# Kernel tuning notes

Measured on AMD Instinct MI355X. Metric: run time of the kernel, lower is better.

The kernel has to match this reference:

```python
import jax, jax.numpy as jnp
import numpy as np

B, W, M, HD, RL, RD = 32, 32, 1024, 64, 2, 32
D = RL * HD  # concat of per-layer hidden states


def setup_inputs() -> dict:
    key = jax.random.key(0)
    ks = jax.random.split(key, 16)
    s = 0.1
    r = lambda k, shape: (jax.random.normal(k, shape, jnp.float32) * s)
    return {
        "x_input": jax.random.normal(ks[0], (B, W, M), jnp.float32),
        "major_graph": jax.random.normal(ks[1], (M, M), jnp.float32) * 0.02,
        "H_init": jnp.zeros((RL, M, HD), jnp.float32),
        # GRU layer 0: input size 1 -> hidden HD
        "Wih0": r(ks[2], (3 * HD, 1)),
        "Whh0": r(ks[3], (3 * HD, HD)),
        "bih0": jnp.zeros((3 * HD,), jnp.float32),
        "bhh0": jnp.zeros((3 * HD,), jnp.float32),
        # GRU layer 1: hidden HD -> hidden HD
        "Wih1": r(ks[4], (3 * HD, HD)),
        "Whh1": r(ks[5], (3 * HD, HD)),
        "bih1": jnp.zeros((3 * HD,), jnp.float32),
        "bhh1": jnp.zeros((3 * HD,), jnp.float32),
        # weight-normed Linear(RL*HD -> RD)
        "V": r(ks[6], (RD, D)),
        "g": jnp.ones((RD,), jnp.float32),
        "b_lin": jnp.zeros((RD,), jnp.float32),
        # FinalRowWise layer: per-node weights [M, RD] -> scalar per node
        "W_fr": r(ks[7], (M, RD)),
        "b_fr": jnp.zeros((M,), jnp.float32),
    }


def _gru_cell(x, h, Wih, Whh, bih, bhh):
    # x: [B, M, in], h: [B, M, HD]
    gi = x @ Wih.T + bih
    gh = h @ Whh.T + bhh
    ir, iz, inn = jnp.split(gi, 3, axis=-1)
    hr, hz, hnn = jnp.split(gh, 3, axis=-1)
    rgate = jax.nn.sigmoid(ir + hr)
    zgate = jax.nn.sigmoid(iz + hz)
    n = jnp.tanh(inn + rgate * hnn)
    return (1.0 - zgate) * n + zgate * h


def reference(x_input, major_graph, H_init, Wih0, Whh0, bih0, bhh0,
              Wih1, Whh1, bih1, bhh1, V, g, b_lin, W_fr, b_fr):
    Bn, Wn_, Mn = x_input.shape
    # h0: [RL, B, M, HD] (H_init broadcast over batch)
    h0 = jnp.broadcast_to(H_init[:, None], (H_init.shape[0], Bn, Mn, H_init.shape[-1]))
    # weight_norm (dim=0): per-output-row normalization of V scaled by g
    Wn = g[:, None] * V / jnp.linalg.norm(V, axis=1, keepdims=True)  # [RD, D]
    x_seq = jnp.transpose(x_input, (1, 0, 2))[..., None]  # [W, B, M, 1]

    def step(hn, x_t):
        hn0 = _gru_cell(x_t, hn, Wih0, Whh0, bih0, bhh0)        # [B, M, HD]
        hn1 = _gru_cell(hn0, h0[1], Wih1, Whh1, bih1, bhh1)     # [B, M, HD] (fresh h0 each step, as in source)
        x_p = jnp.concatenate([hn0, hn1], axis=-1)              # [B, M, D]
        # graph-weighted projection along node axis: x_p @ major_graph
        x_g = jax.nn.relu(jnp.einsum('bid,ij->bjd', x_p, major_graph))  # [B, M, D]
        y = jax.nn.sigmoid(x_g @ Wn.T + b_lin)                  # [B, M, RD]
        out = jnp.einsum('bmd,md->bm', y, W_fr) + b_fr          # [B, M]
        return hn1, out

    _, outs = jax.lax.scan(step, h0[0], x_seq)  # [W, B, M]
    return jnp.transpose(outs, (1, 0, 2))       # [B, W, M]
```

## Files before the change

kernel.cpp:

```cpp
#include <hip/hip_runtime.h>
#include <math.h>

#define B_  32
#define W_  32
#define M_  1024
#define HD_ 64
#define RD_ 32
#define D_  128
#define CH_ 16
#define NKT 16

typedef short bf16x8 __attribute__((ext_vector_type(8)));
typedef float f32x4  __attribute__((ext_vector_type(4)));

#define AS1 __attribute__((address_space(1)))
#define AS3 __attribute__((address_space(3)))

__device__ __forceinline__ void gload16(const void* g, void* l) {
    __builtin_amdgcn_global_load_lds((const AS1 void*)g, (AS3 void*)l, 16, 0, 0);
}

__device__ __forceinline__ unsigned short f2b(float f) {
    unsigned int u = __float_as_uint(f);
    u += 0x7fffu + ((u >> 16) & 1u);
    return (unsigned short)(u >> 16);
}
__device__ __forceinline__ float b2f(unsigned short h) {
    return __uint_as_float(((unsigned int)h) << 16);
}
__device__ __forceinline__ float sigf(float x) { return 1.0f / (1.0f + __expf(-x)); }
__device__ __forceinline__ float tanhf_(float x) { return 2.0f / (1.0f + __expf(-2.0f * x)) - 1.0f; }


__global__ __launch_bounds__(256) void gt_kernel(const float* __restrict__ G,
                                                 unsigned short* __restrict__ GTb) {
    __shared__ float T[64][65];
    int i0 = blockIdx.x * 64, j0 = blockIdx.y * 64;
    int tid = threadIdx.x;
    int r = tid >> 4, c4 = (tid & 15) * 4;
    #pragma unroll
    for (int q = 0; q < 4; ++q) {
        float4 v = *(const float4*)&G[(i0 + r + q * 16) * M_ + j0 + c4];
        T[r + q * 16][c4] = v.x; T[r + q * 16][c4 + 1] = v.y;
        T[r + q * 16][c4 + 2] = v.z; T[r + q * 16][c4 + 3] = v.w;
    }
    __syncthreads();
    #pragma unroll
    for (int q = 0; q < 4; ++q) {
        int jr = r + q * 16;
        ushort4 o;
        o.x = f2b(T[c4][jr]); o.y = f2b(T[c4 + 1][jr]);
        o.z = f2b(T[c4 + 2][jr]); o.w = f2b(T[c4 + 3][jr]);
        *(ushort4*)&GTb[(j0 + jr) * M_ + i0 + c4] = o;
    }
}

__global__ __launch_bounds__(192) void gh1ct_kernel(const float* __restrict__ H_init,
                                                    const float* __restrict__ Whh1,
                                                    const float* __restrict__ bhh1,
                                                    float* __restrict__ gh1cT) {
    int m = blockIdx.x, k = threadIdx.x;
    __shared__ float h01[HD_];
    if (k < HD_) h01[k] = H_init[(M_ + m) * HD_ + k];
    __syncthreads();
    float d = 0.f;
    #pragma unroll
    for (int hd = 0; hd < HD_; ++hd) d = fmaf(h01[hd], Whh1[k * HD_ + hd], d);
    gh1cT[k * M_ + m] = d + bhh1[k];
}

__global__ __launch_bounds__(128) void wn_kernel(const float* __restrict__ V,
                                                 const float* __restrict__ g,
                                                 unsigned short* __restrict__ Wnb) {
    int r = blockIdx.x, d = threadIdx.x;
    float v = V[r * D_ + d];
    float s = v * v;
    #pragma unroll
    for (int off = 32; off > 0; off >>= 1) s += __shfl_down(s, off);
    __shared__ float ws[2];
    if ((threadIdx.x & 63) == 0) ws[threadIdx.x >> 6] = s;
    __syncthreads();
    float norm = sqrtf(ws[0] + ws[1]);
    Wnb[r * D_ + d] = f2b(g[r] * v / norm);
}

__global__ __launch_bounds__(256) void castw_kernel(const float* __restrict__ Whh0,
                                                    const float* __restrict__ Wih1,
                                                    unsigned short* __restrict__ Whh0b,
                                                    unsigned short* __restrict__ Wih1b) {
    int i = blockIdx.x * 256 + threadIdx.x;
    Whh0b[i] = f2b(Whh0[i]);
    Wih1b[i] = f2b(Wih1[i]);
}

__global__ __launch_bounds__(256) void inith_kernel(const float* __restrict__ H_init,
                                                    unsigned short* __restrict__ Hb) {
    int e8 = blockIdx.x * 256 + threadIdx.x;
    int base = e8 * 8;
    int src = base & (M_ * HD_ - 1);
    float4 v0 = *(const float4*)&H_init[src];
    float4 v1 = *(const float4*)&H_init[src + 4];
    uint4 u;
    u.x = (unsigned int)f2b(v0.x) | ((unsigned int)f2b(v0.y) << 16);
    u.y = (unsigned int)f2b(v0.z) | ((unsigned int)f2b(v0.w) << 16);
    u.z = (unsigned int)f2b(v1.x) | ((unsigned int)f2b(v1.y) << 16);
    u.w = (unsigned int)f2b(v1.z) | ((unsigned int)f2b(v1.w) << 16);
    *(uint4*)&Hb[base] = u;
}

__global__ __launch_bounds__(512, 4) void gru_chunk_kernel(
    const float* __restrict__ x_input, const float* __restrict__ Wih0,
    const float* __restrict__ bih0, const float* __restrict__ bhh0,
    const unsigned short* __restrict__ Whh0b, const unsigned short* __restrict__ Wih1b,
    const float* __restrict__ bih1, const float* __restrict__ gh1cT,
    const float* __restrict__ H_init, unsigned short* __restrict__ Hb,
    unsigned short* __restrict__ XPT_c, int t0)
{
    __shared__ unsigned short Whh0s[192 * 64];
    __shared__ unsigned short Wih1s[192 * 64];
    __shared__ unsigned short hn0s[64 * 64];
    __shared__ unsigned short hn1s[64 * 64];
    const int tid = threadIdx.x, w = tid >> 6, l = tid & 63;
    const int li = l & 15, lh = l >> 4;
    const int pg = w >> 1, hf = w & 1;
    const int b = blockIdx.x >> 4, mt = blockIdx.x & 15;
    const int m0 = mt * 64;
    const int p0b = b * M_ + m0;
    const int ms = m0 + pg * 16;

    for (int i = tid; i < 1536; i += 512) {
        int row = i >> 3, pos = i & 7, sc = pos ^ (row & 7);
        gload16(&Whh0b[row * 64 + sc * 8], (char*)Whh0s + (i & ~63) * 16);
        gload16(&Wih1b[row * 64 + sc * 8], (char*)Wih1s + (i & ~63) * 16);
    }
    {
        int p = tid >> 3, cc = tid & 7;
        uint4 v = *(const uint4*)&Hb[(p0b + p) * HD_ + cc * 8];
        *(uint4*)((char*)hn1s + p * 128 + ((cc ^ (p & 7)) << 4)) = v;
    }

    float wi_[3][2], bi0_[3][2], bh0_[3][2], bi1_[3][2];
    float vrA[2][4], vzA[2][4], vnA[2][4], h01A[2][4];
    #pragma unroll
    for (int fi = 0; fi < 2; ++fi) {
        int ko = hf * 32 + fi * 16 + li;
        #pragma unroll
        for (int g3 = 0; g3 < 3; ++g3) {
            wi_[g3][fi]  = Wih0[g3 * 64 + ko];
            bi0_[g3][fi] = bih0[g3 * 64 + ko];
            bh0_[g3][fi] = bhh0[g3 * 64 + ko];
            bi1_[g3][fi] = bih1[g3 * 64 + ko];
        }
        float4 vr = *(const float4*)&gh1cT[(ko) * M_ + ms + lh * 4];
        float4 vz = *(const float4*)&gh1cT[(64 + ko) * M_ + ms + lh * 4];
        float4 vn = *(const float4*)&gh1cT[(128 + ko) * M_ + ms + lh * 4];
        vrA[fi][0] = vr.x; vrA[fi][1] = vr.y; vrA[fi][2] = vr.z; vrA[fi][3] = vr.w;
        vzA[fi][0] = vz.x; vzA[fi][1] = vz.y; vzA[fi][2] = vz.z; vzA[fi][3] = vz.w;
        vnA[fi][0] = vn.x; vnA[fi][1] = vn.y; vnA[fi][2] = vn.z; vnA[fi][3] = vn.w;
        #pragma unroll
        for (int reg = 0; reg < 4; ++reg)
            h01A[fi][reg] = H_init[M_ * HD_ + (ms + lh * 4 + reg) * HD_ + ko];
    }

    __syncthreads();

    float hst[2][4];
    #pragma unroll
    for (int fi = 0; fi < 2; ++fi) {
        int ko = hf * 32 + fi * 16 + li;
        #pragma unroll
        for (int reg = 0; reg < 4; ++reg) {
            int ml = pg * 16 + lh * 4 + reg;
            hst[fi][reg] = b2f(*(const unsigned short*)((char*)hn1s + ml * 128 +
                               ((((ko >> 3) ^ (ml & 7))) << 4) + (ko & 7) * 2));
        }
    }

    for (int ts = 0; ts < CH_; ++ts) {
        int t = t0 + ts;
        float4 xv = *(const float4*)&x_input[(b * W_ + t) * M_ + ms + lh * 4];
        float x4[4] = {xv.x, xv.y, xv.z, xv.w};
        const int rl = pg * 16 + li;

        bf16x8 a0 = *(const bf16x8*)((char*)hn1s + rl * 128 + ((lh ^ (rl & 7)) << 4));
        bf16x8 a1 = *(const bf16x8*)((char*)hn1s + rl * 128 + (((4 + lh) ^ (rl & 7)) << 4));
        f32x4 acc[6];
        #pragma unroll
        for (int q = 0; q < 6; ++q) acc[q] = (f32x4){0.f, 0.f, 0.f, 0.f};
        #pragma unroll
        for (int g3 = 0; g3 < 3; ++g3)
            #pragma unroll
            for (int fi = 0; fi < 2; ++fi) {
                int row = (g3 * 4 + hf * 2 + fi) * 16 + li;
                bf16x8 b0 = *(const bf16x8*)((char*)Whh0s + row * 128 + ((lh ^ (row & 7)) << 4));
                bf16x8 b1 = *(const bf16x8*)((char*)Whh0s + row * 128 + (((4 + lh) ^ (row & 7)) << 4));
                acc[g3 * 2 + fi] = __builtin_amdgcn_mfma_f32_16x16x32_bf16(a0, b0, acc[g3 * 2 + fi], 0, 0, 0);
                acc[g3 * 2 + fi] = __builtin_amdgcn_mfma_f32_16x16x32_bf16(a1, b1, acc[g3 * 2 + fi], 0, 0, 0);
            }
        #pragma unroll
        for (int fi = 0; fi < 2; ++fi) {
            int j = hf * 32 + fi * 16 + li;
            #pragma unroll
            for (int reg = 0; reg < 4; ++reg) {
                int ml = pg * 16 + lh * 4 + reg;
                float x = x4[reg];
                float r = sigf(x * wi_[0][fi] + bi0_[0][fi] + acc[fi][reg]     + bh0_[0][fi]);
                float z = sigf(x * wi_[1][fi] + bi0_[1][fi] + acc[2 + fi][reg] + bh0_[1][fi]);
                float n = tanhf_(x * wi_[2][fi] + bi0_[2][fi] + r * (acc[4 + fi][reg] + bh0_[2][fi]));
                float h0v = (1.f - z) * n + z * hst[fi][reg];
                *(unsigned short*)((char*)hn0s + ml * 128 +
                    ((((j >> 3) ^ (ml & 7))) << 4) + (j & 7) * 2) = f2b(h0v);
            }
        }
        __syncthreads();

        a0 = *(const bf16x8*)((char*)hn0s + rl * 128 + ((lh ^ (rl & 7)) << 4));
        a1 = *(const bf16x8*)((char*)hn0s + rl * 128 + (((4 + lh) ^ (rl & 7)) << 4));
        #pragma unroll
        for (int q = 0; q < 6; ++q) acc[q] = (f32x4){0.f, 0.f, 0.f, 0.f};
        #pragma unroll
        for (int g3 = 0; g3 < 3; ++g3)
            #pragma unroll
            for (int fi = 0; fi < 2; ++fi) {
                int row = (g3 * 4 + hf * 2 + fi) * 16 + li;
                bf16x8 b0 = *(const bf16x8*)((char*)Wih1s + row * 128 + ((lh ^ (row & 7)) << 4));
                bf16x8 b1 = *(const bf16x8*)((char*)Wih1s + row * 128 + (((4 + lh) ^ (row & 7)) << 4));
                acc[g3 * 2 + fi] = __builtin_amdgcn_mfma_f32_16x16x32_bf16(a0, b0, acc[g3 * 2 + fi], 0, 0, 0);
                acc[g3 * 2 + fi] = __builtin_amdgcn_mfma_f32_16x16x32_bf16(a1, b1, acc[g3 * 2 + fi], 0, 0, 0);
            }
        #pragma unroll
        for (int fi = 0; fi < 2; ++fi) {
            int ko = hf * 32 + fi * 16 + li;
            #pragma unroll
            for (int reg = 0; reg < 4; ++reg) {
                int ml = pg * 16 + lh * 4 + reg;
                float r = sigf(acc[fi][reg]     + bi1_[0][fi] + vrA[fi][reg]);
                float z = sigf(acc[2 + fi][reg] + bi1_[1][fi] + vzA[fi][reg]);
                float n = tanhf_(acc[4 + fi][reg] + bi1_[2][fi] + r * vnA[fi][reg]);
                float h1v = (1.f - z) * n + z * h01A[fi][reg];
                hst[fi][reg] = h1v;
                *(unsigned short*)((char*)hn1s + ml * 128 +
                    ((((ko >> 3) ^ (ml & 7))) << 4) + (ko & 7) * 2) = f2b(h1v);
            }
        }
        __syncthreads();

        {
            unsigned short* XPT = XPT_c + (size_t)ts * (D_ * B_ * M_);
            int d = tid >> 2, mh = (tid & 3) * 16;
            const char* src = (d < 64) ? (const char*)hn0s : (const char*)hn1s;
            int dd = d & 63;
            unsigned int pk[8];
            #pragma unroll
            for (int mm = 0; mm < 16; mm += 2) {
                int ma = mh + mm, mb = mh + mm + 1;
                unsigned int ua = *(const unsigned short*)(src + ma * 128 + (((dd >> 3) ^ (ma & 7)) << 4) + (dd & 7) * 2);
                unsigned int ub = *(const unsigned short*)(src + mb * 128 + (((dd >> 3) ^ (mb & 7)) << 4) + (dd & 7) * 2);
                pk[mm >> 1] = ua | (ub << 16);
            }
            uint4 o0 = {pk[0], pk[1], pk[2], pk[3]};
            uint4 o1 = {pk[4], pk[5], pk[6], pk[7]};
            *(uint4*)&XPT[(b * D_ + d) * M_ + m0 + mh]     = o0;
            *(uint4*)&XPT[(b * D_ + d) * M_ + m0 + mh + 8] = o1;
        }
        __syncthreads();
    }

    {
        int p = tid >> 3, cc = tid & 7;
        uint4 v = *(const uint4*)((char*)hn1s + p * 128 + ((cc ^ (p & 7)) << 4));
        *(uint4*)&Hb[(p0b + p) * HD_ + cc * 8] = v;
    }
}

__global__ __launch_bounds__(512, 4) void gemmhead_kernel(
    const unsigned short* __restrict__ GTb, const unsigned short* __restrict__ XPT_c,
    const unsigned short* __restrict__ Wnb, const float* __restrict__ b_lin,
    const float* __restrict__ W_fr, const float* __restrict__ b_fr,
    float* __restrict__ out, int t0)
{
    __shared__ __align__(16) char lds[65536];
    const int tid = threadIdx.x, w = tid >> 6, l = tid & 63;
    const int li = l & 15, lh = l >> 4;
    const int wm = w >> 2, wn = w & 3;
    const int bid = blockIdx.x;
    const int ntile = (bid & 7) + ((bid >> 6) << 3);
    const int j0 = ((bid >> 3) & 7) * 128;
    const unsigned short* Asrc = GTb + (size_t)j0 * M_;
    const unsigned short* Bsrc = XPT_c + (size_t)ntile * 128 * M_;

    f32x4 acc[4][2];
    #pragma unroll
    for (int mi = 0; mi < 4; ++mi)
        #pragma unroll
        for (int ni = 0; ni < 2; ++ni) acc[mi][ni] = (f32x4){0.f, 0.f, 0.f, 0.f};

    #define STAGE(kt, c) { \
        _Pragma("unroll") \
        for (int q = 0; q < 2; ++q) { \
            int i = q * 512 + tid; \
            int row = i >> 3, pos = i & 7, sc = pos ^ (row & 7); \
            gload16(&Asrc[row * M_ + (kt) * 64 + sc * 8], lds + (c) * 32768 + (i & ~63) * 16); \
            gload16(&Bsrc[row * M_ + (kt) * 64 + sc * 8], lds + (c) * 32768 + 16384 + (i & ~63) * 16); \
        } }

    STAGE(0, 0);

    for (int kt = 0; kt < NKT; ++kt) {
        if (kt + 1 < NKT) { STAGE(kt + 1, (kt + 1) & 1);
                            asm volatile("s_waitcnt vmcnt(4)" ::: "memory"); }
        else              { asm volatile("s_waitcnt vmcnt(0)" ::: "memory"); }
        __builtin_amdgcn_s_barrier();
        asm volatile("" ::: "memory");
        const char* Abuf = lds + (kt & 1) * 32768;
        const char* Bbuf = Abuf + 16384;
        bf16x8 af[4][2], bfv[2][2];
        #pragma unroll
        for (int mi = 0; mi < 4; ++mi) {
            int row = wm * 64 + mi * 16 + li;
            #pragma unroll
            for (int kk = 0; kk < 2; ++kk)
                af[mi][kk] = *(const bf16x8*)(Abuf + row * 128 + (((kk * 4 + lh) ^ (row & 7)) << 4));
        }
        #pragma unroll
        for (int ni = 0; ni < 2; ++ni) {
            int row = wn * 32 + ni * 16 + li;
            #pragma unroll
            for (int kk = 0; kk < 2; ++kk)
                bfv[ni][kk] = *(const bf16x8*)(Bbuf + row * 128 + (((kk * 4 + lh) ^ (row & 7)) << 4));
        }
        __builtin_amdgcn_s_setprio(1);
        #pragma unroll
        for (int kk = 0; kk < 2; ++kk)
            #pragma unroll
            for (int mi = 0; mi < 4; ++mi)
                #pragma unroll
                for (int ni = 0; ni < 2; ++ni)
                    acc[mi][ni] = __builtin_amdgcn_mfma_f32_16x16x32_bf16(af[mi][kk], bfv[ni][kk], acc[mi][ni], 0, 0, 0);
        __builtin_amdgcn_s_setprio(0);
        asm volatile("s_waitcnt lgkmcnt(0)" ::: "memory");
        __builtin_amdgcn_s_barrier();
        asm volatile("" ::: "memory");
    }

    __syncthreads();

    #pragma unroll
    for (int mi = 0; mi < 4; ++mi)
        #pragma unroll
        for (int ni = 0; ni < 2; ++ni)
            #pragma unroll
            for (int reg = 0; reg < 4; ++reg) {
                int jl = wm * 64 + mi * 16 + lh * 4 + reg;
                int cl = wn * 32 + ni * 16 + li;
                float v = fmaxf(acc[mi][ni][reg], 0.f);
                int byte = jl * 256 + ((((cl >> 3) ^ (jl & 7))) << 4) + (cl & 7) * 2;
                *(unsigned short*)(lds + byte) = f2b(v);
            }
    __syncthreads();

    const int b = ntile & 31, t = t0 + (ntile >> 5);
    float bl0 = b_lin[li], bl1 = b_lin[16 + li];
    {
        int row = w * 16 + li;
        f32x4 P0 = (f32x4){0.f, 0.f, 0.f, 0.f};
        f32x4 P1 = (f32x4){0.f, 0.f, 0.f, 0.f};
        #pragma unroll
        for (int ks = 0; ks < 4; ++ks) {
            int cp = (ks * 4 + lh) ^ (row & 7);
            bf16x8 xa = *(const bf16x8*)(lds + row * 256 + cp * 16);
            bf16x8 wb0 = *(const bf16x8*)&Wnb[(li) * D_ + ks * 32 + lh * 8];
            bf16x8 wb1 = *(const bf16x8*)&Wnb[(16 + li) * D_ + ks * 32 + lh * 8];
            P0 = __builtin_amdgcn_mfma_f32_16x16x32_bf16(xa, wb0, P0, 0, 0, 0);
            P1 = __builtin_amdgcn_mfma_f32_16x16x32_bf16(xa, wb1, P1, 0, 0, 0);
        }
        float s[4];
        #pragma unroll
        for (int reg = 0; reg < 4; ++reg) {
            int j = j0 + w * 16 + lh * 4 + reg;
            float y0 = sigf(P0[reg] + bl0);
            float y1 = sigf(P1[reg] + bl1);
            s[reg] = y0 * W_fr[j * RD_ + li] + y1 * W_fr[j * RD_ + 16 + li];
        }
        #pragma unroll
        for (int off = 1; off < 16; off <<= 1) {
            #pragma unroll
            for (int reg = 0; reg < 4; ++reg) s[reg] += __shfl_xor(s[reg], off);
        }
        if (li == 0) {
            int jb = j0 + w * 16 + lh * 4;
            float4 o = {s[0] + b_fr[jb], s[1] + b_fr[jb + 1],
                        s[2] + b_fr[jb + 2], s[3] + b_fr[jb + 3]};
            *(float4*)&out[(b * W_ + t) * M_ + jb] = o;
        }
    }
}


extern "C" void kernel_launch(void* const* d_in, const int* in_sizes, int n_in,
                              void* d_out, int out_size, void* d_ws, size_t ws_size,
                              hipStream_t stream) {
    const float* x_input = (const float*)d_in[0];
    const float* G       = (const float*)d_in[1];
    const float* H_init  = (const float*)d_in[2];
    const float* Wih0    = (const float*)d_in[3];
    const float* Whh0    = (const float*)d_in[4];
    const float* bih0    = (const float*)d_in[5];
    const float* bhh0    = (const float*)d_in[6];
    const float* Wih1    = (const float*)d_in[7];
    const float* Whh1    = (const float*)d_in[8];
    const float* bih1    = (const float*)d_in[9];
    const float* bhh1    = (const float*)d_in[10];
    const float* V       = (const float*)d_in[11];
    const float* gvec    = (const float*)d_in[12];
    const float* b_lin   = (const float*)d_in[13];
    const float* W_fr    = (const float*)d_in[14];
    const float* b_fr    = (const float*)d_in[15];
    float* out = (float*)d_out;

    char* ws = (char*)d_ws;
    unsigned short* GTb   = (unsigned short*)(ws);
    unsigned short* XPT_c = (unsigned short*)(ws + (2u   << 20));
    unsigned short* Hb    = (unsigned short*)(ws + (130u << 20));
    float*          gh1cT = (float*)(ws + (134u << 20));
    unsigned short* Wnb   = (unsigned short*)(ws + (135u << 20));
    unsigned short* Whh0b = (unsigned short*)(ws + (135u << 20) + 8192);
    unsigned short* Wih1b = (unsigned short*)(ws + (135u << 20) + 8192 + 24576);

    gt_kernel   <<<dim3(16, 16), 256, 0, stream>>>(G, GTb);
    gh1ct_kernel<<<M_, 192, 0, stream>>>(H_init, Whh1, bhh1, gh1cT);
    wn_kernel   <<<RD_, 128, 0, stream>>>(V, gvec, Wnb);
    castw_kernel<<<48, 256, 0, stream>>>(Whh0, Wih1, Whh0b, Wih1b);
    inith_kernel<<<1024, 256, 0, stream>>>(H_init, Hb);

    for (int c = 0; c < W_ / CH_; ++c) {
        gru_chunk_kernel<<<512, 512, 0, stream>>>(x_input, Wih0, bih0, bhh0, Whh0b,
                                                  Wih1b, bih1, gh1cT, H_init, Hb,
                                                  XPT_c, c * CH_);
        gemmhead_kernel<<<dim3(4096), 512, 0, stream>>>(GTb, XPT_c, Wnb, b_lin,
                                                        W_fr, b_fr, out, c * CH_);
    }
}
```

Before: 586.5 us.

## Double-buffer GRU hidden LDS and enlarge gemmhead tile to 256 rows

The GRU chunk kernel now ping-pongs its hn0/hn1 LDS buffers by timestep parity, which removes the trailing barrier in each step. The graph GEMM+head kernel now uses a 256-row output tile with BK=32 and 4x4 MFMA fragments per wave, and the grid is halved. The larger tile raises reuse of the XPT operand and halves the number of blocks and redundant head epilogues. The trade-offs are higher register pressure and a K loop with twice as many iterations. Removing the barrier relies on parity buffering being enough to prevent read/write races between consecutive steps.

```diff
diff --git a/kernel.cpp b/kernel.cpp
--- a/kernel.cpp
+++ b/kernel.cpp
@@ -8,7 +8,6 @@
 #define RD_ 32
 #define D_  128
 #define CH_ 16
-#define NKT 16
 
 typedef short bf16x8 __attribute__((ext_vector_type(8)));
 typedef float f32x4  __attribute__((ext_vector_type(4)));
@@ -118,8 +117,8 @@
 {
     __shared__ unsigned short Whh0s[192 * 64];
     __shared__ unsigned short Wih1s[192 * 64];
-    __shared__ unsigned short hn0s[64 * 64];
-    __shared__ unsigned short hn1s[64 * 64];
+    __shared__ unsigned short hn0s[2][64 * 64];
+    __shared__ unsigned short hn1s[2][64 * 64];
     const int tid = threadIdx.x, w = tid >> 6, l = tid & 63;
     const int li = l & 15, lh = l >> 4;
     const int pg = w >> 1, hf = w & 1;
@@ -136,7 +135,7 @@
     {
         int p = tid >> 3, cc = tid & 7;
         uint4 v = *(const uint4*)&Hb[(p0b + p) * HD_ + cc * 8];
-        *(uint4*)((char*)hn1s + p * 128 + ((cc ^ (p & 7)) << 4)) = v;
+        *(uint4*)((char*)hn1s[1] + p * 128 + ((cc ^ (p & 7)) << 4)) = v;
     }
 
     float wi_[3][2], bi0_[3][2], bh0_[3][2], bi1_[3][2];
@@ -171,19 +170,20 @@
         #pragma unroll
         for (int reg = 0; reg < 4; ++reg) {
             int ml = pg * 16 + lh * 4 + reg;
-            hst[fi][reg] = b2f(*(const unsigned short*)((char*)hn1s + ml * 128 +
+            hst[fi][reg] = b2f(*(const unsigned short*)((char*)hn1s[1] + ml * 128 +
                                ((((ko >> 3) ^ (ml & 7))) << 4) + (ko & 7) * 2));
         }
     }
 
     for (int ts = 0; ts < CH_; ++ts) {
         int t = t0 + ts;
+        const int X = ts & 1, Xp = X ^ 1;
         float4 xv = *(const float4*)&x_input[(b * W_ + t) * M_ + ms + lh * 4];
         float x4[4] = {xv.x, xv.y, xv.z, xv.w};
         const int rl = pg * 16 + li;
 
-        bf16x8 a0 = *(const bf16x8*)((char*)hn1s + rl * 128 + ((lh ^ (rl & 7)) << 4));
-        bf16x8 a1 = *(const bf16x8*)((char*)hn1s + rl * 128 + (((4 + lh) ^ (rl & 7)) << 4));
+        bf16x8 a0 = *(const bf16x8*)((char*)hn1s[Xp] + rl * 128 + ((lh ^ (rl & 7)) << 4));
+        bf16x8 a1 = *(const bf16x8*)((char*)hn1s[Xp] + rl * 128 + (((4 + lh) ^ (rl & 7)) << 4));
         f32x4 acc[6];
         #pragma unroll
         for (int q = 0; q < 6; ++q) acc[q] = (f32x4){0.f, 0.f, 0.f, 0.f};
@@ -208,14 +208,14 @@
                 float z = sigf(x * wi_[1][fi] + bi0_[1][fi] + acc[2 + fi][reg] + bh0_[1][fi]);
                 float n = tanhf_(x * wi_[2][fi] + bi0_[2][fi] + r * (acc[4 + fi][reg] + bh0_[2][fi]));
                 float h0v = (1.f - z) * n + z * hst[fi][reg];
-                *(unsigned short*)((char*)hn0s + ml * 128 +
+                *(unsigned short*)((char*)hn0s[X] + ml * 128 +
                     ((((j >> 3) ^ (ml & 7))) << 4) + (j & 7) * 2) = f2b(h0v);
             }
         }
         __syncthreads();
 
-        a0 = *(const bf16x8*)((char*)hn0s + rl * 128 + ((lh ^ (rl & 7)) << 4));
-        a1 = *(const bf16x8*)((char*)hn0s + rl * 128 + (((4 + lh) ^ (rl & 7)) << 4));
+        a0 = *(const bf16x8*)((char*)hn0s[X] + rl * 128 + ((lh ^ (rl & 7)) << 4));
+        a1 = *(const bf16x8*)((char*)hn0s[X] + rl * 128 + (((4 + lh) ^ (rl & 7)) << 4));
         #pragma unroll
         for (int q = 0; q < 6; ++q) acc[q] = (f32x4){0.f, 0.f, 0.f, 0.f};
         #pragma unroll
@@ -239,7 +239,7 @@
                 float n = tanhf_(acc[4 + fi][reg] + bi1_[2][fi] + r * vnA[fi][reg]);
                 float h1v = (1.f - z) * n + z * h01A[fi][reg];
                 hst[fi][reg] = h1v;
-                *(unsigned short*)((char*)hn1s + ml * 128 +
+                *(unsigned short*)((char*)hn1s[X] + ml * 128 +
                     ((((ko >> 3) ^ (ml & 7))) << 4) + (ko & 7) * 2) = f2b(h1v);
             }
         }
@@ -248,7 +248,7 @@
         {
             unsigned short* XPT = XPT_c + (size_t)ts * (D_ * B_ * M_);
             int d = tid >> 2, mh = (tid & 3) * 16;
-            const char* src = (d < 64) ? (const char*)hn0s : (const char*)hn1s;
+            const char* src = (d < 64) ? (const char*)hn0s[X] : (const char*)hn1s[X];
             int dd = d & 63;
             unsigned int pk[8];
             #pragma unroll
@@ -263,12 +263,11 @@
             *(uint4*)&XPT[(b * D_ + d) * M_ + m0 + mh]     = o0;
             *(uint4*)&XPT[(b * D_ + d) * M_ + m0 + mh + 8] = o1;
         }
-        __syncthreads();
     }
 
     {
         int p = tid >> 3, cc = tid & 7;
-        uint4 v = *(const uint4*)((char*)hn1s + p * 128 + ((cc ^ (p & 7)) << 4));
+        uint4 v = *(const uint4*)((char*)hn1s[1] + p * 128 + ((cc ^ (p & 7)) << 4));
         *(uint4*)&Hb[(p0b + p) * HD_ + cc * 8] = v;
     }
 }
@@ -282,61 +281,58 @@
     __shared__ __align__(16) char lds[65536];
     const int tid = threadIdx.x, w = tid >> 6, l = tid & 63;
     const int li = l & 15, lh = l >> 4;
-    const int wm = w >> 2, wn = w & 3;
+    const int wm = w >> 1, wn = w & 1;
     const int bid = blockIdx.x;
-    const int ntile = (bid & 7) + ((bid >> 6) << 3);
-    const int j0 = ((bid >> 3) & 7) * 128;
+    const int ntile = bid >> 2;
+    const int j0 = (bid & 3) * 256;
     const unsigned short* Asrc = GTb + (size_t)j0 * M_;
     const unsigned short* Bsrc = XPT_c + (size_t)ntile * 128 * M_;
 
-    f32x4 acc[4][2];
+    f32x4 acc[4][4];
     #pragma unroll
     for (int mi = 0; mi < 4; ++mi)
         #pragma unroll
-        for (int ni = 0; ni < 2; ++ni) acc[mi][ni] = (f32x4){0.f, 0.f, 0.f, 0.f};
-
-    #define STAGE(kt, c) { \
+        for (int ni = 0; ni < 4; ++ni) acc[mi][ni] = (f32x4){0.f, 0.f, 0.f, 0.f};
+
+    #define GSTAGE(kt, c) { \
         _Pragma("unroll") \
         for (int q = 0; q < 2; ++q) { \
             int i = q * 512 + tid; \
-            int row = i >> 3, pos = i & 7, sc = pos ^ (row & 7); \
-            gload16(&Asrc[row * M_ + (kt) * 64 + sc * 8], lds + (c) * 32768 + (i & ~63) * 16); \
-            gload16(&Bsrc[row * M_ + (kt) * 64 + sc * 8], lds + (c) * 32768 + 16384 + (i & ~63) * 16); \
-        } }
-
-    STAGE(0, 0);
-
-    for (int kt = 0; kt < NKT; ++kt) {
-        if (kt + 1 < NKT) { STAGE(kt + 1, (kt + 1) & 1);
-                            asm volatile("s_waitcnt vmcnt(4)" ::: "memory"); }
-        else              { asm volatile("s_waitcnt vmcnt(0)" ::: "memory"); }
+            int row = i >> 2, pos = i & 3, sc = pos ^ (row & 3); \
+            gload16(&Asrc[row * M_ + (kt) * 32 + sc * 8], lds + (c) * 24576 + (i & ~63) * 16); \
+        } \
+        { int i = tid; \
+          int row = i >> 2, pos = i & 3, sc = pos ^ (row & 3); \
+          gload16(&Bsrc[row * M_ + (kt) * 32 + sc * 8], lds + (c) * 24576 + 16384 + (i & ~63) * 16); } \
+    }
+
+    GSTAGE(0, 0);
+
+    for (int kt = 0; kt < 32; ++kt) {
+        if (kt + 1 < 32) { GSTAGE(kt + 1, (kt + 1) & 1);
+                           asm volatile("s_waitcnt vmcnt(3)" ::: "memory"); }
+        else             { asm volatile("s_waitcnt vmcnt(0)" ::: "memory"); }
         __builtin_amdgcn_s_barrier();
         asm volatile("" ::: "memory");
-        const char* Abuf = lds + (kt & 1) * 32768;
+        const char* Abuf = lds + (kt & 1) * 24576;
         const char* Bbuf = Abuf + 16384;
-        bf16x8 af[4][2], bfv[2][2];
+        bf16x8 af[4], bfv[4];
         #pragma unroll
         for (int mi = 0; mi < 4; ++mi) {
             int row = wm * 64 + mi * 16 + li;
-            #pragma unroll
-            for (int kk = 0; kk < 2; ++kk)
-                af[mi][kk] = *(const bf16x8*)(Abuf + row * 128 + (((kk * 4 + lh) ^ (row & 7)) << 4));
-        }
-        #pragma unroll
-        for (int ni = 0; ni < 2; ++ni) {
-            int row = wn * 32 + ni * 16 + li;
-            #pragma unroll
-            for (int kk = 0; kk < 2; ++kk)
-                bfv[ni][kk] = *(const bf16x8*)(Bbuf + row * 128 + (((kk * 4 + lh) ^ (row & 7)) << 4));
+            af[mi] = *(const bf16x8*)(Abuf + row * 64 + ((lh ^ (row & 3)) << 4));
+        }
+        #pragma unroll
+        for (int ni = 0; ni < 4; ++ni) {
+            int row = wn * 64 + ni * 16 + li;
+            bfv[ni] = *(const bf16x8*)(Bbuf + row * 64 + ((lh ^ (row & 3)) << 4));
         }
         __builtin_amdgcn_s_setprio(1);
         #pragma unroll
-        for (int kk = 0; kk < 2; ++kk)
-            #pragma unroll
-            for (int mi = 0; mi < 4; ++mi)
-                #pragma unroll
-                for (int ni = 0; ni < 2; ++ni)
-                    acc[mi][ni] = __builtin_amdgcn_mfma_f32_16x16x32_bf16(af[mi][kk], bfv[ni][kk], acc[mi][ni], 0, 0, 0);
+        for (int mi = 0; mi < 4; ++mi)
+            #pragma unroll
+            for (int ni = 0; ni < 4; ++ni)
+                acc[mi][ni] = __builtin_amdgcn_mfma_f32_16x16x32_bf16(af[mi], bfv[ni], acc[mi][ni], 0, 0, 0);
         __builtin_amdgcn_s_setprio(0);
         asm volatile("s_waitcnt lgkmcnt(0)" ::: "memory");
         __builtin_amdgcn_s_barrier();
@@ -348,11 +344,11 @@
     #pragma unroll
     for (int mi = 0; mi < 4; ++mi)
         #pragma unroll
-        for (int ni = 0; ni < 2; ++ni)
+        for (int ni = 0; ni < 4; ++ni)
             #pragma unroll
             for (int reg = 0; reg < 4; ++reg) {
                 int jl = wm * 64 + mi * 16 + lh * 4 + reg;
-                int cl = wn * 32 + ni * 16 + li;
+                int cl = wn * 64 + ni * 16 + li;
                 float v = fmaxf(acc[mi][ni][reg], 0.f);
                 int byte = jl * 256 + ((((cl >> 3) ^ (jl & 7))) << 4) + (cl & 7) * 2;
                 *(unsigned short*)(lds + byte) = f2b(v);
@@ -361,8 +357,9 @@
 
     const int b = ntile & 31, t = t0 + (ntile >> 5);
     float bl0 = b_lin[li], bl1 = b_lin[16 + li];
-    {
-        int row = w * 16 + li;
+    #pragma unroll
+    for (int rg = 0; rg < 2; ++rg) {
+        int row = w * 32 + rg * 16 + li;
         f32x4 P0 = (f32x4){0.f, 0.f, 0.f, 0.f};
         f32x4 P1 = (f32x4){0.f, 0.f, 0.f, 0.f};
         #pragma unroll
@@ -377,7 +374,7 @@
         float s[4];
         #pragma unroll
         for (int reg = 0; reg < 4; ++reg) {
-            int j = j0 + w * 16 + lh * 4 + reg;
+            int j = j0 + w * 32 + rg * 16 + lh * 4 + reg;
             float y0 = sigf(P0[reg] + bl0);
             float y1 = sigf(P1[reg] + bl1);
             s[reg] = y0 * W_fr[j * RD_ + li] + y1 * W_fr[j * RD_ + 16 + li];
@@ -388,7 +385,7 @@
             for (int reg = 0; reg < 4; ++reg) s[reg] += __shfl_xor(s[reg], off);
         }
         if (li == 0) {
-            int jb = j0 + w * 16 + lh * 4;
+            int jb = j0 + w * 32 + rg * 16 + lh * 4;
             float4 o = {s[0] + b_fr[jb], s[1] + b_fr[jb + 1],
                         s[2] + b_fr[jb + 2], s[3] + b_fr[jb + 3]};
             *(float4*)&out[(b * W_ + t) * M_ + jb] = o;
@@ -437,7 +434,7 @@
         gru_chunk_kernel<<<512, 512, 0, stream>>>(x_input, Wih0, bih0, bhh0, Whh0b,
                                                   Wih1b, bih1, gh1cT, H_init, Hb,
                                                   XPT_c, c * CH_);
-        gemmhead_kernel<<<dim3(4096), 512, 0, stream>>>(GTb, XPT_c, Wnb, b_lin,
+        gemmhead_kernel<<<dim3(2048), 512, 0, stream>>>(GTb, XPT_c, Wnb, b_lin,
                                                         W_fr, b_fr, out, c * CH_);
     }
 }
```

New measurement: 620.3 us. +5.8%, slower.
